# Kernel tuning notes

Measured on AMD Instinct MI355X. Metric: run time of the kernel, lower is better.

Reference implementation:

```python
import jax, jax.numpy as jnp
import numpy as np

STACK_DEPTH = 16
SHARPEN = 5.0
LN_EPS = 1e-5
EPS = 1e-8


def _apply_tools(x, tw):
    # tools: relu, gelu(exact), tanh, sigmoid, identity; tw: [B, 5]
    return (jax.nn.relu(x) * tw[:, 0:1]
            + jax.nn.gelu(x, approximate=False) * tw[:, 1:2]
            + jnp.tanh(x) * tw[:, 2:3]
            + jax.nn.sigmoid(x) * tw[:, 3:4]
            + x * tw[:, 4:5])


def _forward(hidden_states, W_proj, b_proj, W_op, b_op, W_tool, b_tool, ln_gamma, ln_beta):
    B, S, H = hidden_states.shape
    D = STACK_DEPTH

    # Per-timestep linear ops are time-independent -> batch them up front.
    proj = jnp.einsum('bsh,ph->bsp', hidden_states, W_proj) + b_proj  # [B,S,2H]
    h_all, v_all = proj[..., :H], proj[..., H:]
    op_probs = jax.nn.softmax(jnp.einsum('bsh,oh->bso', hidden_states, W_op) + b_op, axis=-1)  # [B,S,3]
    tool_w = jax.nn.softmax(jnp.einsum('bsh,th->bst', h_all, W_tool) + b_tool, axis=-1)  # [B,S,T]

    # Differentiable stack recurrence (push/pop/nop with pointer sharpening).
    stack0 = jnp.zeros((B, D, H), hidden_states.dtype)
    pointer0 = jnp.zeros((B, D), hidden_states.dtype).at[:, 0].set(1.0)

    def step(carry, xs):
        stack, pointer = carry
        value, ops = xs  # value: [B,H], ops: [B,3]
        push, pop, nop = ops[:, 0:1], ops[:, 1:2], ops[:, 2:3]
        p_push = jnp.roll(pointer, 1, axis=1)   # pointer moves up on push
        p_pop = jnp.roll(pointer, -1, axis=1)   # pointer moves down on pop
        new_p = push * p_push + pop * p_pop + nop * pointer
        new_p = new_p ** SHARPEN
        new_p = new_p / (jnp.sum(new_p, axis=1, keepdims=True) + EPS)
        w = (push * p_push)[..., None]          # [B,D,1] write weight at pushed slot
        new_stack = stack * (1.0 - w) + value[:, None, :] * w
        top = jnp.sum(new_stack * new_p[..., None], axis=1)  # [B,H]
        return (new_stack, new_p), top

    (stack_f, pointer_f), tops = jax.lax.scan(
        step, (stack0, pointer0),
        (jnp.swapaxes(v_all, 0, 1), jnp.swapaxes(op_probs, 0, 1)))
    tops = jnp.swapaxes(tops, 0, 1)  # [B,S,H]

    processed = jax.vmap(_apply_tools, in_axes=(1, 1), out_axes=1)(tops, tool_w)  # [B,S,H]
    combined = h_all + processed + hidden_states

    mu = jnp.mean(combined, axis=-1, keepdims=True)
    var = jnp.mean((combined - mu) ** 2, axis=-1, keepdims=True)
    final = (combined - mu) * jax.lax.rsqrt(var + LN_EPS) * ln_gamma + ln_beta
    return final, stack_f, pointer_f, tool_w


def setup_inputs() -> dict:
    key = jax.random.key(0)
    ks = jax.random.split(key, 4)
    B, S, H, T = 16, 2048, 1024, 5
    sd = 1.0 / np.sqrt(H)
    return {
        'hidden_states': jax.random.normal(ks[0], (B, S, H), jnp.float32),
        'W_proj': jax.random.normal(ks[1], (2 * H, H), jnp.float32) * sd,
        'b_proj': jnp.zeros((2 * H,), jnp.float32),
        'W_op': jax.random.normal(ks[2], (3, H), jnp.float32) * sd,
        'b_op': jnp.zeros((3,), jnp.float32),
        'W_tool': jax.random.normal(ks[3], (T, H), jnp.float32) * sd,
        'b_tool': jnp.zeros((T,), jnp.float32),
        'ln_gamma': jnp.ones((H,), jnp.float32),
        'ln_beta': jnp.zeros((H,), jnp.float32),
    }


def reference(hidden_states, W_proj, b_proj, W_op, b_op, W_tool, b_tool, ln_gamma, ln_beta):
    return _forward(hidden_states, W_proj, b_proj, W_op, b_op, W_tool, b_tool, ln_gamma, ln_beta)
```

## Files before the change

kernel.cpp:

```cpp
#include <hip/hip_runtime.h>
#include <hip/hip_bf16.h>
#include <cstdint>
#include <cstdio>


typedef float f32x4 __attribute__((ext_vector_type(4)));
typedef __bf16 bf8v __attribute__((ext_vector_type(8)));

#define WS_ABF   0ULL
#define WS_WBF   67108864ULL
#define WS_PROJ  71303168ULL
#define WS_OP4   205520896ULL
#define WS_WP    206045184ULL
#define WS_NEED  210239488ULL

#define OUT_FINAL 0
#define OUT_STACK 33554432ULL
#define OUT_PTR   33816576ULL
#define OUT_TOOLW 33816832ULL
#define SLE_OFF    0ULL
#define SSTART_OFF 9437184ULL
#define ATOT_OFF   30000000ULL

__device__ __forceinline__ float bf2f(unsigned short u) {
    union { unsigned int i; float f; } v; v.i = ((unsigned int)u) << 16; return v.f;
}
__device__ __forceinline__ unsigned short f2bf(float f) {
    __hip_bfloat16 h = __float2bfloat16(f);
    return __builtin_bit_cast(unsigned short, h);
}
template<int C>
__device__ __forceinline__ float fdpp(float x) {
    return __int_as_float(__builtin_amdgcn_mov_dpp(__float_as_int(x), C, 0xF, 0xF, true));
}
__device__ __forceinline__ void gload_lds16(const void* g, void* l) {
    __builtin_amdgcn_global_load_lds(
        (__attribute__((address_space(1))) void*)(uintptr_t)g,
        (__attribute__((address_space(3))) void*)l,
        16, 0, 0);
}

__global__ __launch_bounds__(256) void k0(const float* __restrict__ hid,
                                          const float* __restrict__ Wp,
                                          const float* __restrict__ Wop,
                                          const float* __restrict__ bop,
                                          unsigned short* __restrict__ Abf,
                                          unsigned short* __restrict__ Wbf,
                                          float4* __restrict__ op4)
{
    const int bid = blockIdx.x, tid = threadIdx.x;
    if (bid < 8192) {
        const int wid = tid >> 6, lane = tid & 63;
        const int row = bid * 4 + wid;
        const float* hrow = hid + (size_t)row * 1024 + lane * 16;
        float xs[16];
        #pragma unroll
        for (int j = 0; j < 4; ++j) {
            float4 t = *(const float4*)(hrow + j * 4);
            xs[j*4+0] = t.x; xs[j*4+1] = t.y; xs[j*4+2] = t.z; xs[j*4+3] = t.w;
        }
        unsigned short us[16];
        #pragma unroll
        for (int j = 0; j < 16; ++j) us[j] = f2bf(xs[j]);
        uint4 ulo, uhi;
        ulo.x = (unsigned)us[0]  | ((unsigned)us[1]  << 16);
        ulo.y = (unsigned)us[2]  | ((unsigned)us[3]  << 16);
        ulo.z = (unsigned)us[4]  | ((unsigned)us[5]  << 16);
        ulo.w = (unsigned)us[6]  | ((unsigned)us[7]  << 16);
        uhi.x = (unsigned)us[8]  | ((unsigned)us[9]  << 16);
        uhi.y = (unsigned)us[10] | ((unsigned)us[11] << 16);
        uhi.z = (unsigned)us[12] | ((unsigned)us[13] << 16);
        uhi.w = (unsigned)us[14] | ((unsigned)us[15] << 16);
        unsigned short* arow = Abf + (size_t)row * 1024 + lane * 16;
        *(uint4*)(arow)     = ulo;
        *(uint4*)(arow + 8) = uhi;
        float pt[3] = {0.f, 0.f, 0.f};
        #pragma unroll
        for (int o = 0; o < 3; ++o) {
            const float* wrow = Wop + o * 1024 + lane * 16;
            #pragma unroll
            for (int j = 0; j < 4; ++j) {
                float4 t = *(const float4*)(wrow + j * 4);
                pt[o] += xs[j*4+0]*t.x + xs[j*4+1]*t.y + xs[j*4+2]*t.z + xs[j*4+3]*t.w;
            }
        }
        #pragma unroll
        for (int o = 0; o < 3; ++o)
            #pragma unroll
            for (int m = 32; m >= 1; m >>= 1) pt[o] += __shfl_xor(pt[o], m);
        if (lane == 0) {
            float l0 = pt[0] + bop[0], l1 = pt[1] + bop[1], l2 = pt[2] + bop[2];
            float mx = fmaxf(l0, fmaxf(l1, l2));
            float e0 = expf(l0 - mx), e1 = expf(l1 - mx), e2 = expf(l2 - mx);
            float inv = 1.0f / (e0 + e1 + e2);
            float4 r; r.x = e0 * inv; r.y = e1 * inv; r.z = e2 * inv; r.w = 0.f;
            op4[row] = r;
        }
    } else {
        const int b2 = bid - 8192;
        const size_t base = (size_t)b2 * 2048 + tid * 8;
        float4 a = *(const float4*)(Wp + base);
        float4 b = *(const float4*)(Wp + base + 4);
        unsigned short vs[8] = { f2bf(a.x), f2bf(a.y), f2bf(a.z), f2bf(a.w),
                                 f2bf(b.x), f2bf(b.y), f2bf(b.z), f2bf(b.w) };
        uint4 u;
        u.x = (unsigned)vs[0] | ((unsigned)vs[1] << 16);
        u.y = (unsigned)vs[2] | ((unsigned)vs[3] << 16);
        u.z = (unsigned)vs[4] | ((unsigned)vs[5] << 16);
        u.w = (unsigned)vs[6] | ((unsigned)vs[7] << 16);
        *(uint4*)(Wbf + base) = u;
    }
}

__global__ __launch_bounds__(512, 2) void k1(const unsigned short* __restrict__ Abf,
                                             const unsigned short* __restrict__ Wbf,
                                             const float* __restrict__ bproj,
                                             unsigned short* __restrict__ proj,
                                             const float4* __restrict__ op4,
                                             float* __restrict__ wpbuf,
                                             float* __restrict__ out)
{
    __shared__ uint4 sm[8192];
    const int bid = blockIdx.x, tid = threadIdx.x;

    if (bid < 16) {
        const int b = bid;
        #pragma unroll
        for (int i = 0; i < 4; ++i)
            sm[tid + i * 512] = ((const uint4*)op4)[(size_t)b * 2048 + tid + i * 512];
        __syncthreads();
        if (tid >= 64) return;
        __builtin_amdgcn_s_setprio(1);
        const int lane = tid, d = lane & 15;
        const float probe = (float)d;
        const bool ror1_is_push = (fdpp<0x121>(probe) == (float)((d + 15) & 15));
        float p = (d == 0) ? 1.0f : 0.0f;
        float Apre = 1.0f;
        const float4* smf = (const float4*)sm;
        float4 o0 = smf[0], o1 = smf[1];
        float* wpb = wpbuf + (size_t)b * 2048 * 32;
        float* atot = out + ATOT_OFF + (size_t)b * 32 * 16;
        #pragma unroll 2
        for (int s = 0; s < 2048; ++s) {
            float4 o2 = smf[(s + 2 < 2048) ? (s + 2) : 2047];
            const float push = o0.x, pop = o0.y, nop = o0.z;
            const float ra = fdpp<0x121>(p);
            const float rb = fdpp<0x12F>(p);
            const float ppush = ror1_is_push ? ra : rb;
            const float ppop  = ror1_is_push ? rb : ra;
            const float w = push * ppush;
            float lin = push * ppush + pop * ppop + nop * p;
            float x2 = lin * lin;
            float x5 = x2 * x2 * lin;
            float sum = x5;
            sum += fdpp<0x128>(sum);
            sum += fdpp<0x124>(sum);
            sum += fdpp<0x122>(sum);
            sum += fdpp<0x121>(sum);
            float pn = x5 * __builtin_amdgcn_rcpf(sum + 1e-8f);
            const float om = 1.0f - w;
            Apre = ((s & 63) == 0) ? om : Apre * om;
            if (lane < 16) {
                float2 wp; wp.x = w; wp.y = pn;
                *(float2*)(wpb + ((size_t)s * 16 + d) * 2) = wp;
                if ((s & 63) == 63) atot[(s >> 6) * 16 + d] = Apre;
            }
            p = pn;
            o0 = o1; o1 = o2;
        }
        if (lane < 16) out[OUT_PTR + (size_t)b * 16 + d] = p;
        return;
    }

    const int li = bid - 16;
    const int xcd = li & 7, j = li >> 3;
    const int gm = xcd * 16 + (j >> 3);
    const int gn = j & 7;
    const int wid = tid >> 6, lane = tid & 63;
    const int wm = wid >> 2, wn = wid & 3;
    const size_t row0 = (size_t)gm * 256;
    const size_t col0 = (size_t)gn * 256;
    char* smc = (char*)sm;
    const char* Ab = (const char*)Abf;
    const char* Bb = (const char*)Wbf;
    const int laneR = lane & 15;
    const int laneK = (lane >> 4) * 16;

    f32x4 acc[8][4];
    const f32x4 z = {0.f, 0.f, 0.f, 0.f};
    #pragma unroll
    for (int i = 0; i < 8; ++i)
        #pragma unroll
        for (int jj = 0; jj < 4; ++jj) acc[i][jj] = z;

    auto STAGE = [&](int kt, int slot) {
        #pragma unroll
        for (int hf = 0; hf < 4; ++hf) {
            #pragma unroll
            for (int i = 0; i < 2; ++i) {
                const int idx  = i * 512 + tid;
                const int off  = idx * 16;
                const int soff = off ^ (((off >> 7) & 7) << 4);
                const int irow = soff >> 7;
                const int colb = soff & 127;
                const char* src = (hf < 2)
                    ? (Ab + (row0 + (size_t)(hf * 128 + irow)) * 2048 + (size_t)kt * 128 + colb)
                    : (Bb + (col0 + (size_t)((hf - 2) * 128 + irow)) * 2048 + (size_t)kt * 128 + colb);
                gload_lds16(src, smc + slot * 65536 + hf * 16384 + (i * 512 + wid * 64) * 16);
            }
        }
    };

    STAGE(0, 0);
    int cur = 0;
    #pragma unroll 1
    for (int kt = 0; kt < 16; ++kt) {
        if (kt < 15) {
            STAGE(kt + 1, cur ^ 1);
            asm volatile("s_waitcnt vmcnt(8)" ::: "memory");
        } else {
            asm volatile("s_waitcnt vmcnt(0)" ::: "memory");
        }
        __builtin_amdgcn_sched_barrier(0);
        __builtin_amdgcn_s_barrier();
        const char* Abase = smc + cur * 65536 + wm * 16384;
        const char* Bbase = smc + cur * 65536 + 32768 + (wn >> 1) * 16384;
        const int bro = (wn & 1) * 64;

        bf8v af[4][2], bfr[4][2];
        #pragma unroll
        for (int m2 = 0; m2 < 4; ++m2)
            #pragma unroll
            for (int kk = 0; kk < 2; ++kk) {
                int byt = (m2 * 16 + laneR) * 128 + kk * 64 + laneK;
                byt ^= ((byt >> 7) & 7) << 4;
                af[m2][kk] = *(const bf8v*)(Abase + byt);
            }
        #pragma unroll
        for (int n2 = 0; n2 < 2; ++n2)
            #pragma unroll
            for (int kk = 0; kk < 2; ++kk) {
                int byt = (bro + n2 * 16 + laneR) * 128 + kk * 64 + laneK;
                byt ^= ((byt >> 7) & 7) << 4;
                bfr[n2][kk] = *(const bf8v*)(Bbase + byt);
            }
        __builtin_amdgcn_s_setprio(1);
        #pragma unroll
        for (int m2 = 0; m2 < 4; ++m2)
            #pragma unroll
            for (int n2 = 0; n2 < 2; ++n2)
                #pragma unroll
                for (int kk = 0; kk < 2; ++kk)
                    acc[m2][n2] = __builtin_amdgcn_mfma_f32_16x16x32_bf16(af[m2][kk], bfr[n2][kk], acc[m2][n2], 0, 0, 0);
        __builtin_amdgcn_s_setprio(0);
        __builtin_amdgcn_s_barrier();
        #pragma unroll
        for (int n2 = 2; n2 < 4; ++n2)
            #pragma unroll
            for (int kk = 0; kk < 2; ++kk) {
                int byt = (bro + n2 * 16 + laneR) * 128 + kk * 64 + laneK;
                byt ^= ((byt >> 7) & 7) << 4;
                bfr[n2][kk] = *(const bf8v*)(Bbase + byt);
            }
        __builtin_amdgcn_s_setprio(1);
        #pragma unroll
        for (int m2 = 0; m2 < 4; ++m2)
            #pragma unroll
            for (int n2 = 2; n2 < 4; ++n2)
                #pragma unroll
                for (int kk = 0; kk < 2; ++kk)
                    acc[m2][n2] = __builtin_amdgcn_mfma_f32_16x16x32_bf16(af[m2][kk], bfr[n2][kk], acc[m2][n2], 0, 0, 0);
        __builtin_amdgcn_s_setprio(0);
        __builtin_amdgcn_s_barrier();
        #pragma unroll
        for (int m2 = 0; m2 < 4; ++m2)
            #pragma unroll
            for (int kk = 0; kk < 2; ++kk) {
                int byt = ((64 + m2 * 16 + laneR)) * 128 + kk * 64 + laneK;
                byt ^= ((byt >> 7) & 7) << 4;
                af[m2][kk] = *(const bf8v*)(Abase + byt);
            }
        __builtin_amdgcn_s_setprio(1);
        #pragma unroll
        for (int m2 = 0; m2 < 4; ++m2)
            #pragma unroll
            for (int n2 = 2; n2 < 4; ++n2)
                #pragma unroll
                for (int kk = 0; kk < 2; ++kk)
                    acc[4 + m2][n2] = __builtin_amdgcn_mfma_f32_16x16x32_bf16(af[m2][kk], bfr[n2][kk], acc[4 + m2][n2], 0, 0, 0);
        __builtin_amdgcn_s_setprio(0);
        __builtin_amdgcn_s_barrier();
        __builtin_amdgcn_s_setprio(1);
        #pragma unroll
        for (int m2 = 0; m2 < 4; ++m2)
            #pragma unroll
            for (int n2 = 0; n2 < 2; ++n2)
                #pragma unroll
                for (int kk = 0; kk < 2; ++kk)
                    acc[4 + m2][n2] = __builtin_amdgcn_mfma_f32_16x16x32_bf16(af[m2][kk], bfr[n2][kk], acc[4 + m2][n2], 0, 0, 0);
        __builtin_amdgcn_s_setprio(0);
        __builtin_amdgcn_s_barrier();
        cur ^= 1;
    }
    #pragma unroll
    for (int mr = 0; mr < 8; ++mr) {
        const int rloc = wm * 128 + mr * 16 + ((lane >> 4) * 4);
        #pragma unroll
        for (int nr = 0; nr < 4; ++nr) {
            const size_t col = col0 + wn * 64 + nr * 16 + laneR;
            const float bias = bproj[col];
            #pragma unroll
            for (int jj = 0; jj < 4; ++jj)
                proj[(row0 + rloc + jj) * 2048 + col] = f2bf(acc[mr][nr][jj] + bias);
        }
    }
}

__global__ __launch_bounds__(256) void k2(const unsigned short* __restrict__ proj,
                                          const float* __restrict__ wpbuf,
                                          float* __restrict__ sle)
{
    __shared__ unsigned short vlds[2][4096];
    const int bid = blockIdx.x, tid = threadIdx.x;
    const int hg = bid & 3, c = (bid >> 2) & 31, b = bid >> 7;
    if (c == 31) return;
    const int wid = tid >> 6;
    const char* vbase = (const char*)proj +
        ((size_t)(b * 2048 + c * 64) * 2048 + 1024 + hg * 256) * 2;
    const float* wpb = wpbuf + ((size_t)b * 2048 + c * 64) * 32;

    float st[16];
    #pragma unroll
    for (int d = 0; d < 16; ++d) st[d] = 0.f;

    auto STAGE = [&](int sc, int buf) {
        #pragma unroll
        for (int i = 0; i < 2; ++i) {
            const int g = i * 256 + tid;
            gload_lds16(vbase + (size_t)(sc * 16 + (g >> 5)) * 4096 + (g & 31) * 16,
                        (char*)vlds + buf * 8192 + (i * 256 + wid * 64) * 16);
        }
    };
    STAGE(0, 0);
    __syncthreads();
    for (int sc = 0; sc < 4; ++sc) {
        const int cur = sc & 1;
        if (sc < 3) STAGE(sc + 1, cur ^ 1);
        const unsigned short* vl = vlds[cur];
        #pragma unroll 4
        for (int ls = 0; ls < 16; ++ls) {
            const float v = bf2f(vl[ls * 256 + tid]);
            const float4* wp4 = (const float4*)(wpb + (size_t)(sc * 16 + ls) * 32);
            #pragma unroll
            for (int k = 0; k < 8; ++k) {
                float4 q = wp4[k];
                st[2*k]   = fmaf(q.x, v - st[2*k],   st[2*k]);
                st[2*k+1] = fmaf(q.z, v - st[2*k+1], st[2*k+1]);
            }
        }
        __syncthreads();
    }
    float* so = sle + ((size_t)b * 32 + c) * 16 * 1024 + hg * 256 + tid;
    #pragma unroll
    for (int d = 0; d < 16; ++d) so[(size_t)d * 1024] = st[d];
}

__global__ __launch_bounds__(256) void k2b(const float* __restrict__ sle,
                                           const float* __restrict__ atot,
                                           float* __restrict__ sstart)
{
    const int bid = blockIdx.x, tid = threadIdx.x;
    const int hg = bid & 3, d = (bid >> 2) & 15, b = bid >> 6;
    const int h = hg * 256 + tid;
    const float* sb = sle    + ((size_t)b * 512 + d) * 1024 + h;
    float*       so = sstart + ((size_t)b * 512 + d) * 1024 + h;
    const float* ab = atot + (size_t)b * 512 + d;
    float st = 0.f;
    #pragma unroll 4
    for (int c = 0; c < 31; ++c) {
        so[(size_t)c * 16384] = st;
        st = fmaf(ab[c * 16], st, sb[(size_t)c * 16384]);
    }
    so[31ull * 16384] = st;
}

__global__ __launch_bounds__(256) void k3(unsigned short* __restrict__ proj,
                                          const float* __restrict__ wpbuf,
                                          const float* __restrict__ sstart,
                                          float* __restrict__ out)
{
    __shared__ unsigned short vlds[2][4096];
    const int bid = blockIdx.x, tid = threadIdx.x;
    const int hg = bid & 3, c = (bid >> 2) & 31, b = bid >> 7;
    const int wid = tid >> 6;
    const char* vbase = (const char*)proj +
        ((size_t)(b * 2048 + c * 64) * 2048 + 1024 + hg * 256) * 2;
    const float* wpb = wpbuf + ((size_t)b * 2048 + c * 64) * 32;

    float st[16];
    {
        const float* ss = sstart + ((size_t)b * 32 + c) * 16 * 1024 + hg * 256 + tid;
        #pragma unroll
        for (int d = 0; d < 16; ++d) st[d] = ss[(size_t)d * 1024];
    }

    unsigned short* topb = proj + ((size_t)b * 2048 + c * 64) * 2048 + 1024 + hg * 256 + tid;

    auto STAGE = [&](int sc, int buf) {
        #pragma unroll
        for (int i = 0; i < 2; ++i) {
            const int g = i * 256 + tid;
            gload_lds16(vbase + (size_t)(sc * 16 + (g >> 5)) * 4096 + (g & 31) * 16,
                        (char*)vlds + buf * 8192 + (i * 256 + wid * 64) * 16);
        }
    };
    STAGE(0, 0);
    __syncthreads();
    for (int sc = 0; sc < 4; ++sc) {
        const int cur = sc & 1;
        if (sc < 3) STAGE(sc + 1, cur ^ 1);
        const unsigned short* vl = vlds[cur];
        #pragma unroll 4
        for (int ls = 0; ls < 16; ++ls) {
            const float v = bf2f(vl[ls * 256 + tid]);
            const float4* wp4 = (const float4*)(wpb + (size_t)(sc * 16 + ls) * 32);
            float t0 = 0.f, t1 = 0.f;
            #pragma unroll
            for (int k = 0; k < 8; ++k) {
                float4 q = wp4[k];
                st[2*k]   = fmaf(q.x, v - st[2*k],   st[2*k]);
                st[2*k+1] = fmaf(q.z, v - st[2*k+1], st[2*k+1]);
                t0 = fmaf(q.y, st[2*k],   t0);
                t1 = fmaf(q.w, st[2*k+1], t1);
            }
            topb[(size_t)(sc * 16 + ls) * 2048] = f2bf(t0 + t1);
        }
        __syncthreads();
    }
    if (c == 31) {
        #pragma unroll
        for (int d = 0; d < 16; ++d)
            out[OUT_STACK + ((size_t)b * 16 + d) * 1024 + hg * 256 + tid] = st[d];
    }
}

__global__ __launch_bounds__(256) void k5(const unsigned short* __restrict__ proj,
                                          const unsigned short* __restrict__ hidbf,
                                          const float* __restrict__ Wtool,
                                          const float* __restrict__ btool,
                                          const float* __restrict__ gamma,
                                          const float* __restrict__ beta,
                                          float* __restrict__ out)
{
    __shared__ float red[4][8];
    const int row = blockIdx.x, tid = threadIdx.x;
    const int wid = tid >> 6, lane = tid & 63;
    const int k0i = tid * 4;
    uint2 hu = *(const uint2*)(proj + (size_t)row * 2048 + k0i);
    float hh[4];
    hh[0] = bf2f(hu.x & 0xffff); hh[1] = bf2f(hu.x >> 16);
    hh[2] = bf2f(hu.y & 0xffff); hh[3] = bf2f(hu.y >> 16);
    uint2 tu = *(const uint2*)(proj + (size_t)row * 2048 + 1024 + k0i);
    float xs[4];
    xs[0] = bf2f(tu.x & 0xffff); xs[1] = bf2f(tu.x >> 16);
    xs[2] = bf2f(tu.y & 0xffff); xs[3] = bf2f(tu.y >> 16);
    uint2 du = *(const uint2*)(hidbf + (size_t)row * 1024 + k0i);
    float hds[4];
    hds[0] = bf2f(du.x & 0xffff); hds[1] = bf2f(du.x >> 16);
    hds[2] = bf2f(du.y & 0xffff); hds[3] = bf2f(du.y >> 16);
    float pt[5];
    #pragma unroll
    for (int t = 0; t < 5; ++t) {
        float4 wv = *(const float4*)(Wtool + t * 1024 + k0i);
        pt[t] = hh[0]*wv.x + hh[1]*wv.y + hh[2]*wv.z + hh[3]*wv.w;
    }
    #pragma unroll
    for (int t = 0; t < 5; ++t)
        #pragma unroll
        for (int m = 32; m >= 1; m >>= 1) pt[t] += __shfl_xor(pt[t], m);
    if (lane == 0) {
        #pragma unroll
        for (int t = 0; t < 5; ++t) red[wid][t] = pt[t];
    }
    __syncthreads();
    float tw[5];
    {
        float lg[5];
        #pragma unroll
        for (int t = 0; t < 5; ++t)
            lg[t] = red[0][t] + red[1][t] + red[2][t] + red[3][t] + btool[t];
        float mx = fmaxf(fmaxf(fmaxf(lg[0], lg[1]), fmaxf(lg[2], lg[3])), lg[4]);
        float se = 0.f;
        #pragma unroll
        for (int t = 0; t < 5; ++t) { tw[t] = expf(lg[t] - mx); se += tw[t]; }
        float inv = 1.0f / se;
        #pragma unroll
        for (int t = 0; t < 5; ++t) tw[t] *= inv;
    }
    if (tid < 5) out[OUT_TOOLW + (size_t)row * 5 + tid] = tw[tid];
    float cj[4];
    #pragma unroll
    for (int j = 0; j < 4; ++j) {
        const float x = xs[j];
        const float rl = fmaxf(x, 0.f);
        const float gl = 0.5f * x * (1.f + erff(x * 0.70710678118654752f));
        const float th = tanhf(x);
        const float sg = 1.f / (1.f + expf(-x));
        const float pr = rl*tw[0] + gl*tw[1] + th*tw[2] + sg*tw[3] + x*tw[4];
        cj[j] = hh[j] + pr + hds[j];
    }
    float s1 = cj[0] + cj[1] + cj[2] + cj[3];
    float s2 = cj[0]*cj[0] + cj[1]*cj[1] + cj[2]*cj[2] + cj[3]*cj[3];
    #pragma unroll
    for (int m = 32; m >= 1; m >>= 1) { s1 += __shfl_xor(s1, m); s2 += __shfl_xor(s2, m); }
    __syncthreads();
    if (lane == 0) { red[wid][0] = s1; red[wid][1] = s2; }
    __syncthreads();
    const float S1 = red[0][0] + red[1][0] + red[2][0] + red[3][0];
    const float S2 = red[0][1] + red[1][1] + red[2][1] + red[3][1];
    const float mu = S1 * (1.f / 1024.f);
    const float var = S2 * (1.f / 1024.f) - mu * mu;
    const float rstd = rsqrtf(var + 1e-5f);
    float4 g4 = *(const float4*)(gamma + k0i);
    float4 b4 = *(const float4*)(beta + k0i);
    float4 res;
    res.x = (cj[0] - mu) * rstd * g4.x + b4.x;
    res.y = (cj[1] - mu) * rstd * g4.y + b4.y;
    res.z = (cj[2] - mu) * rstd * g4.z + b4.z;
    res.w = (cj[3] - mu) * rstd * g4.w + b4.w;
    *(float4*)(out + (size_t)row * 1024 + k0i) = res;
}

extern "C" void kernel_launch(void* const* d_in, const int* in_sizes, int n_in,
                              void* d_out, int out_size, void* d_ws, size_t ws_size,
                              hipStream_t stream)
{
    if (ws_size < WS_NEED) {
        fprintf(stderr, "kernel_launch: ws_size %zu < required %llu\n",
                ws_size, (unsigned long long)WS_NEED);
        return;
    }
    const float* hid = (const float*)d_in[0];
    const float* Wp  = (const float*)d_in[1];
    const float* bp  = (const float*)d_in[2];
    const float* Wop = (const float*)d_in[3];
    const float* bop = (const float*)d_in[4];
    const float* Wtl = (const float*)d_in[5];
    const float* btl = (const float*)d_in[6];
    const float* gam = (const float*)d_in[7];
    const float* bet = (const float*)d_in[8];
    float* out = (float*)d_out;
    char* ws = (char*)d_ws;
    unsigned short* Abf  = (unsigned short*)(ws + WS_ABF);
    unsigned short* Wbf  = (unsigned short*)(ws + WS_WBF);
    unsigned short* proj = (unsigned short*)(ws + WS_PROJ);
    float4* op4 = (float4*)(ws + WS_OP4);
    float* wpbuf = (float*)(ws + WS_WP);
    float* sle    = out + SLE_OFF;
    float* sstart = out + SSTART_OFF;
    float* atot   = out + ATOT_OFF;

    k0<<<9216, 256, 0, stream>>>(hid, Wp, Wop, bop, Abf, Wbf, op4);
    k1<<<1040, 512, 0, stream>>>(Abf, Wbf, bp, proj, op4, wpbuf, out);
    k2<<<2048, 256, 0, stream>>>(proj, wpbuf, sle);
    k2b<<<1024, 256, 0, stream>>>(sle, atot, sstart);
    k3<<<2048, 256, 0, stream>>>(proj, wpbuf, sstart, out);
    k5<<<32768, 256, 0, stream>>>(proj, Abf, Wtl, btl, gam, bet, out);
}
```

Measured before the change: 517.6 us.

## Replace recurrence replay with linear carry-in correction after local chunk scan

The chunked stack scan now runs once, from zero state, and writes both the local top values and the chunk-end states. A small kernel computes per-step decay coefficients for each chunk. A final kernel adds the carried-in start state, scaled by those coefficients, to the local tops instead of replaying the whole recurrence a second time. This removes one full pass over the value tensor and its serial FMA chain, at the cost of an extra launch, an in-place bf16 round trip on the tops, and 64KB of LDS per block in the correction kernel.

```diff
diff --git a/kernel.cpp b/kernel.cpp
--- a/kernel.cpp
+++ b/kernel.cpp
@@ -20,6 +20,7 @@
 #define OUT_TOOLW 33816832ULL
 #define SLE_OFF    0ULL
 #define SSTART_OFF 9437184ULL
+#define COEF_OFF   18874368ULL
 #define ATOT_OFF   30000000ULL
 
 __device__ __forceinline__ float bf2f(unsigned short u) {
@@ -316,78 +317,9 @@
     }
 }
 
-__global__ __launch_bounds__(256) void k2(const unsigned short* __restrict__ proj,
+__global__ __launch_bounds__(256) void k2(unsigned short* __restrict__ proj,
                                           const float* __restrict__ wpbuf,
                                           float* __restrict__ sle)
-{
-    __shared__ unsigned short vlds[2][4096];
-    const int bid = blockIdx.x, tid = threadIdx.x;
-    const int hg = bid & 3, c = (bid >> 2) & 31, b = bid >> 7;
-    if (c == 31) return;
-    const int wid = tid >> 6;
-    const char* vbase = (const char*)proj +
-        ((size_t)(b * 2048 + c * 64) * 2048 + 1024 + hg * 256) * 2;
-    const float* wpb = wpbuf + ((size_t)b * 2048 + c * 64) * 32;
-
-    float st[16];
-    #pragma unroll
-    for (int d = 0; d < 16; ++d) st[d] = 0.f;
-
-    auto STAGE = [&](int sc, int buf) {
-        #pragma unroll
-        for (int i = 0; i < 2; ++i) {
-            const int g = i * 256 + tid;
-            gload_lds16(vbase + (size_t)(sc * 16 + (g >> 5)) * 4096 + (g & 31) * 16,
-                        (char*)vlds + buf * 8192 + (i * 256 + wid * 64) * 16);
-        }
-    };
-    STAGE(0, 0);
-    __syncthreads();
-    for (int sc = 0; sc < 4; ++sc) {
-        const int cur = sc & 1;
-        if (sc < 3) STAGE(sc + 1, cur ^ 1);
-        const unsigned short* vl = vlds[cur];
-        #pragma unroll 4
-        for (int ls = 0; ls < 16; ++ls) {
-            const float v = bf2f(vl[ls * 256 + tid]);
-            const float4* wp4 = (const float4*)(wpb + (size_t)(sc * 16 + ls) * 32);
-            #pragma unroll
-            for (int k = 0; k < 8; ++k) {
-                float4 q = wp4[k];
-                st[2*k]   = fmaf(q.x, v - st[2*k],   st[2*k]);
-                st[2*k+1] = fmaf(q.z, v - st[2*k+1], st[2*k+1]);
-            }
-        }
-        __syncthreads();
-    }
-    float* so = sle + ((size_t)b * 32 + c) * 16 * 1024 + hg * 256 + tid;
-    #pragma unroll
-    for (int d = 0; d < 16; ++d) so[(size_t)d * 1024] = st[d];
-}
-
-__global__ __launch_bounds__(256) void k2b(const float* __restrict__ sle,
-                                           const float* __restrict__ atot,
-                                           float* __restrict__ sstart)
-{
-    const int bid = blockIdx.x, tid = threadIdx.x;
-    const int hg = bid & 3, d = (bid >> 2) & 15, b = bid >> 6;
-    const int h = hg * 256 + tid;
-    const float* sb = sle    + ((size_t)b * 512 + d) * 1024 + h;
-    float*       so = sstart + ((size_t)b * 512 + d) * 1024 + h;
-    const float* ab = atot + (size_t)b * 512 + d;
-    float st = 0.f;
-    #pragma unroll 4
-    for (int c = 0; c < 31; ++c) {
-        so[(size_t)c * 16384] = st;
-        st = fmaf(ab[c * 16], st, sb[(size_t)c * 16384]);
-    }
-    so[31ull * 16384] = st;
-}
-
-__global__ __launch_bounds__(256) void k3(unsigned short* __restrict__ proj,
-                                          const float* __restrict__ wpbuf,
-                                          const float* __restrict__ sstart,
-                                          float* __restrict__ out)
 {
     __shared__ unsigned short vlds[2][4096];
     const int bid = blockIdx.x, tid = threadIdx.x;
@@ -396,15 +328,11 @@
     const char* vbase = (const char*)proj +
         ((size_t)(b * 2048 + c * 64) * 2048 + 1024 + hg * 256) * 2;
     const float* wpb = wpbuf + ((size_t)b * 2048 + c * 64) * 32;
+    unsigned short* topb = proj + ((size_t)b * 2048 + c * 64) * 2048 + 1024 + hg * 256 + tid;
 
     float st[16];
-    {
-        const float* ss = sstart + ((size_t)b * 32 + c) * 16 * 1024 + hg * 256 + tid;
-        #pragma unroll
-        for (int d = 0; d < 16; ++d) st[d] = ss[(size_t)d * 1024];
-    }
-
-    unsigned short* topb = proj + ((size_t)b * 2048 + c * 64) * 2048 + 1024 + hg * 256 + tid;
+    #pragma unroll
+    for (int d = 0; d < 16; ++d) st[d] = 0.f;
 
     auto STAGE = [&](int sc, int buf) {
         #pragma unroll
@@ -437,10 +365,102 @@
         }
         __syncthreads();
     }
+    float* so = sle + ((size_t)b * 32 + c) * 16 * 1024 + hg * 256 + tid;
+    #pragma unroll
+    for (int d = 0; d < 16; ++d) so[(size_t)d * 1024] = st[d];
+}
+
+__global__ __launch_bounds__(64) void k2c(const float* __restrict__ wpbuf,
+                                          float* __restrict__ coefb)
+{
+    const int bid = blockIdx.x, tid = threadIdx.x;
+    if (tid >= 16) return;
+    const int b = bid >> 5, c = bid & 31;
+    const float* wp = wpbuf + (size_t)b * 65536 + (size_t)c * 64 * 32 + tid * 2;
+    float* co = coefb + (size_t)bid * 1024 + tid;
+    float A = 1.f;
+    #pragma unroll 8
+    for (int j = 0; j < 64; ++j) {
+        float2 q = *(const float2*)(wp + j * 32);
+        A *= (1.f - q.x);
+        co[j * 16] = q.y * A;
+    }
+}
+
+__global__ __launch_bounds__(256) void k2b(const float* __restrict__ sle,
+                                           const float* __restrict__ atot,
+                                           float* __restrict__ sstart)
+{
+    const int bid = blockIdx.x, tid = threadIdx.x;
+    const int hg = bid & 3, d = (bid >> 2) & 15, b = bid >> 6;
+    const int h = hg * 256 + tid;
+    const float* sb = sle    + ((size_t)b * 512 + d) * 1024 + h;
+    float*       so = sstart + ((size_t)b * 512 + d) * 1024 + h;
+    const float* ab = atot + (size_t)b * 512 + d;
+    float st = 0.f;
+    #pragma unroll 4
+    for (int c = 0; c < 31; ++c) {
+        so[(size_t)c * 16384] = st;
+        st = fmaf(ab[c * 16], st, sb[(size_t)c * 16384]);
+    }
+    so[31ull * 16384] = st;
+}
+
+__global__ __launch_bounds__(256) void k3p(unsigned short* __restrict__ proj,
+                                           const float* __restrict__ sstart,
+                                           const float* __restrict__ coefb,
+                                           const float* __restrict__ sle,
+                                           const float* __restrict__ atot,
+                                           float* __restrict__ out)
+{
+    __shared__ float ssL[16384];
+    __shared__ float cofL[1024];
+    const int bid = blockIdx.x, tid = threadIdx.x;
+    const int b = bid >> 5, c = bid & 31;
+    {
+        const float4* ssg = (const float4*)(sstart + (size_t)bid * 16384);
+        #pragma unroll
+        for (int i = 0; i < 16; ++i)
+            ((float4*)ssL)[i * 256 + tid] = ssg[i * 256 + tid];
+        ((float4*)cofL)[tid] = ((const float4*)(coefb + (size_t)bid * 1024))[tid];
+    }
+    __syncthreads();
+    const int h0 = tid * 4;
+    float ss[16][4];
+    #pragma unroll
+    for (int d = 0; d < 16; ++d) {
+        float4 t = *(const float4*)(ssL + d * 1024 + h0);
+        ss[d][0] = t.x; ss[d][1] = t.y; ss[d][2] = t.z; ss[d][3] = t.w;
+    }
+    unsigned short* trow = proj + ((size_t)(b * 2048 + c * 64)) * 2048 + 1024 + h0;
+    #pragma unroll 2
+    for (int s = 0; s < 64; ++s) {
+        uint2 tu = *(const uint2*)(trow + (size_t)s * 2048);
+        float a0 = bf2f(tu.x & 0xffff), a1 = bf2f(tu.x >> 16);
+        float a2 = bf2f(tu.y & 0xffff), a3 = bf2f(tu.y >> 16);
+        #pragma unroll
+        for (int d = 0; d < 16; ++d) {
+            const float cf = cofL[s * 16 + d];
+            a0 = fmaf(cf, ss[d][0], a0);
+            a1 = fmaf(cf, ss[d][1], a1);
+            a2 = fmaf(cf, ss[d][2], a2);
+            a3 = fmaf(cf, ss[d][3], a3);
+        }
+        uint2 o;
+        o.x = (unsigned)f2bf(a0) | ((unsigned)f2bf(a1) << 16);
+        o.y = (unsigned)f2bf(a2) | ((unsigned)f2bf(a3) << 16);
+        *(uint2*)(trow + (size_t)s * 2048) = o;
+    }
     if (c == 31) {
         #pragma unroll
-        for (int d = 0; d < 16; ++d)
-            out[OUT_STACK + ((size_t)b * 16 + d) * 1024 + hg * 256 + tid] = st[d];
+        for (int d = 0; d < 16; ++d) {
+            float4 sl = *(const float4*)(sle + (((size_t)b * 32 + 31) * 16 + d) * 1024 + h0);
+            const float A = atot[(size_t)b * 512 + 31 * 16 + d];
+            float4 r;
+            r.x = fmaf(A, ss[d][0], sl.x); r.y = fmaf(A, ss[d][1], sl.y);
+            r.z = fmaf(A, ss[d][2], sl.z); r.w = fmaf(A, ss[d][3], sl.w);
+            *(float4*)(out + OUT_STACK + ((size_t)b * 16 + d) * 1024 + h0) = r;
+        }
     }
 }
 
@@ -558,12 +578,14 @@
     float* wpbuf = (float*)(ws + WS_WP);
     float* sle    = out + SLE_OFF;
     float* sstart = out + SSTART_OFF;
+    float* coefb  = out + COEF_OFF;
     float* atot   = out + ATOT_OFF;
 
-    k0<<<9216, 256, 0, stream>>>(hid, Wp, Wop, bop, Abf, Wbf, op4);
-    k1<<<1040, 512, 0, stream>>>(Abf, Wbf, bp, proj, op4, wpbuf, out);
-    k2<<<2048, 256, 0, stream>>>(proj, wpbuf, sle);
+    k0 <<<9216, 256, 0, stream>>>(hid, Wp, Wop, bop, Abf, Wbf, op4);
+    k1 <<<1040, 512, 0, stream>>>(Abf, Wbf, bp, proj, op4, wpbuf, out);
+    k2 <<<2048, 256, 0, stream>>>(proj, wpbuf, sle);
+    k2c<<<512,  64,  0, stream>>>(wpbuf, coefb);
     k2b<<<1024, 256, 0, stream>>>(sle, atot, sstart);
-    k3<<<2048, 256, 0, stream>>>(proj, wpbuf, sstart, out);
-    k5<<<32768, 256, 0, stream>>>(proj, Abf, Wtl, btl, gam, bet, out);
-}
+    k3p<<<512,  256, 0, stream>>>(proj, sstart, coefb, sle, atot, out);
+    k5 <<<32768, 256, 0, stream>>>(proj, Abf, Wtl, btl, gam, bet, out);
+}
```

Result: faster. 473.6 us (-8.5%).
